# Performance work log

Hardware: AMD Instinct MI355X
Metric: run time of the kernel (lower is better)

## Reference

```python
import jax, jax.numpy as jnp
import numpy as np

DIM = 512
NUM_HEADS = 8
HEAD_DIM = DIM // NUM_HEADS
SCALE = HEAD_DIM ** -0.5


def setup_inputs() -> dict:
    key = jax.random.key(0)
    ks = jax.random.split(key, 11)
    B, T, D = 2, 4096, DIM
    s = 0.02
    return {
        "query": jax.random.normal(ks[0], (B, T, D), jnp.float32),
        "key_": jax.random.normal(ks[1], (B, T, D), jnp.float32),
        "value": jax.random.normal(ks[2], (B, T, D), jnp.float32),
        "Wq": jax.random.normal(ks[3], (D, D), jnp.float32) * s,
        "bq": jnp.zeros((D,), jnp.float32),
        "Wk": jax.random.normal(ks[4], (D, D), jnp.float32) * s,
        "bk": jnp.zeros((D,), jnp.float32),
        "Wv": jax.random.normal(ks[5], (D, D), jnp.float32) * s,
        "bv": jnp.zeros((D,), jnp.float32),
        "Wo": jax.random.normal(ks[6], (D, D), jnp.float32) * s,
        "bo": jnp.zeros((D,), jnp.float32),
    }


def reference(query, key_, value, Wq, bq, Wk, bk, Wv, bv, Wo, bo):
    B, T, D = query.shape
    H, Hd = NUM_HEADS, HEAD_DIM
    # Linear projections (torch Linear: x @ W.T + b)
    q = (query @ Wq.T + bq).reshape(B, T, H, Hd).transpose(0, 2, 1, 3)   # [B,H,T,Hd]
    k = (key_ @ Wk.T + bk).reshape(B, -1, H, Hd).transpose(0, 2, 1, 3)    # [B,H,S,Hd]
    v = (value @ Wv.T + bv).reshape(B, -1, H, Hd).transpose(0, 2, 1, 3)   # [B,H,S,Hd]
    # Full O(T*S) score matrix, as in the original (non-fused) module
    scores = jnp.einsum("bhtd,bhsd->bhts", q, k) * SCALE                  # [B,H,T,S]
    weights = jax.nn.softmax(scores, axis=-1)
    out = jnp.einsum("bhts,bhsd->bhtd", weights, v)                       # [B,H,T,Hd]
    out = out.transpose(0, 2, 1, 3).reshape(B, T, D)
    return out @ Wo.T + bo
```

## Files before the change

### kernel.cpp

```cpp
#include <hip/hip_runtime.h>
#include <cstdint>
#include <cstddef>

typedef __attribute__((ext_vector_type(8)))  __bf16 bf16x8;
typedef __attribute__((ext_vector_type(4)))  float  f32x4;
typedef __attribute__((ext_vector_type(16))) float  f32x16;
typedef __attribute__((ext_vector_type(8)))  unsigned short us8;

#define MFMA(a, b, c)   __builtin_amdgcn_mfma_f32_16x16x32_bf16((a), (b), (c), 0, 0, 0)
#define MFMA32(a, b, c) __builtin_amdgcn_mfma_f32_32x32x16_bf16((a), (b), (c), 0, 0, 0)

#define QSCALE 0.18033688011112042f

__device__ __forceinline__ unsigned short f2bf(float f) {
  unsigned u = __float_as_uint(f);
  u += 0x7fffu + ((u >> 16) & 1u);
  return (unsigned short)(u >> 16);
}

__device__ __forceinline__ float bf2f(unsigned short s) {
  unsigned u = ((unsigned)s) << 16;
  return __uint_as_float(u);
}

__device__ __forceinline__ unsigned cvtpk(float lo, float hi) {
  unsigned r;
  asm("v_cvt_pk_bf16_f32 %0, %1, %2" : "=v"(r) : "v"(lo), "v"(hi));
  return r;
}

__device__ __forceinline__ void pl32swap(unsigned& a, unsigned& b) {
  asm("v_permlane32_swap_b32 %0, %1" : "+v"(a), "+v"(b));
}

__device__ __forceinline__ void gload16(const void* g, void* l) {
  __builtin_amdgcn_global_load_lds(
      (__attribute__((address_space(1))) unsigned int*)(uintptr_t)g,
      (__attribute__((address_space(3))) unsigned int*)l,
      16, 0, 0);
}

__device__ __forceinline__ float tree16(const float* p) {
  float a = (p[0] + p[1]) + (p[2] + p[3]);
  float b = (p[4] + p[5]) + (p[6] + p[7]);
  float c = (p[8] + p[9]) + (p[10] + p[11]);
  float d = (p[12] + p[13]) + (p[14] + p[15]);
  return (a + b) + (c + d);
}

struct CastArgs {
  const float*    src[7];
  unsigned short* dst[7];
  int             n4[7];
};
__global__ __launch_bounds__(256) void cast_kernel(CastArgs a) {
  int z = blockIdx.y;
  const float* __restrict__ in = a.src[z];
  unsigned short* __restrict__ out = a.dst[z];
  int i = blockIdx.x * 256 + threadIdx.x;
  if (i < a.n4[z]) {
    float4 f = ((const float4*)in)[i];
    ushort4 r;
    r.x = f2bf(f.x); r.y = f2bf(f.y); r.z = f2bf(f.z); r.w = f2bf(f.w);
    ((ushort4*)out)[i] = r;
  }
}

struct ProjArgs {
  const unsigned short* X[3];
  const unsigned short* W[3];
  const float*          bias[3];
  unsigned short*       out[3];
};

__global__ __launch_bounds__(256) void proj_qkv_kernel(ProjArgs args) {
  __shared__ alignas(16) unsigned short smem[16384];

  const int z = blockIdx.z;
  const unsigned short* __restrict__ X   = args.X[z];
  const unsigned short* __restrict__ W   = args.W[z];
  const float* __restrict__ bias         = args.bias[z];
  unsigned short* __restrict__ out       = args.out[z];
  const float scl = (z == 0) ? QSCALE : 1.0f;

  const int t = threadIdx.x;
  const int w = t >> 6, lane = t & 63;
  const int quad = lane >> 4, l15 = lane & 15;
  const int wr = w >> 1, wc = w & 1;
  const int m0 = blockIdx.x * 128, n0 = blockIdx.y * 128;

  const int srow = t >> 2;
  const int scol = (((t & 3) ^ (srow & 3)) << 3);

  f32x4 acc[4][4] = {};

  {
    unsigned short* sA = smem;
    unsigned short* sB = smem + 4096;
    gload16(X + (size_t)(m0 + srow) * 512 + scol,      &sA[w * 512]);
    gload16(X + (size_t)(m0 + srow + 64) * 512 + scol, &sA[2048 + w * 512]);
    gload16(W + (size_t)(n0 + srow) * 512 + scol,      &sB[w * 512]);
    gload16(W + (size_t)(n0 + srow + 64) * 512 + scol, &sB[2048 + w * 512]);
  }

  for (int k0 = 0; k0 < 512; k0 += 32) {
    const int buf = (k0 >> 5) & 1;
    unsigned short* sA = smem + buf * 8192;
    unsigned short* sB = sA + 4096;
    if (k0 < 480) {
      unsigned short* nA = smem + (buf ^ 1) * 8192;
      unsigned short* nB = nA + 4096;
      const int kn = k0 + 32;
      gload16(X + (size_t)(m0 + srow) * 512 + kn + scol,      &nA[w * 512]);
      gload16(X + (size_t)(m0 + srow + 64) * 512 + kn + scol, &nA[2048 + w * 512]);
      gload16(W + (size_t)(n0 + srow) * 512 + kn + scol,      &nB[w * 512]);
      gload16(W + (size_t)(n0 + srow + 64) * 512 + kn + scol, &nB[2048 + w * 512]);
      asm volatile("s_waitcnt vmcnt(4)" ::: "memory");
    } else {
      asm volatile("s_waitcnt vmcnt(0)" ::: "memory");
    }
    __builtin_amdgcn_s_barrier();
    asm volatile("" ::: "memory");

    bf16x8 af[4], bfr[4];
#pragma unroll
    for (int mt = 0; mt < 4; ++mt) {
      int ra = wr * 64 + mt * 16 + l15;
      af[mt] = *(const bf16x8*)&sA[ra * 32 + ((quad ^ (ra & 3)) << 3)];
    }
#pragma unroll
    for (int nt = 0; nt < 4; ++nt) {
      int rb = wc * 64 + nt * 16 + l15;
      bfr[nt] = *(const bf16x8*)&sB[rb * 32 + ((quad ^ (rb & 3)) << 3)];
    }
#pragma unroll
    for (int mt = 0; mt < 4; ++mt)
#pragma unroll
      for (int nt = 0; nt < 4; ++nt)
        acc[mt][nt] = MFMA(af[mt], bfr[nt], acc[mt][nt]);

    asm volatile("" ::: "memory");
    __builtin_amdgcn_s_barrier();
  }

  if (z != 2) {
#pragma unroll
    for (int nt = 0; nt < 4; ++nt) {
      int n = n0 + wc * 64 + nt * 16 + l15;
      float bv = bias[n];
      int h = n >> 6, hd = n & 63;
#pragma unroll
      for (int mt = 0; mt < 4; ++mt) {
#pragma unroll
        for (int r = 0; r < 4; ++r) {
          int m = m0 + wr * 64 + mt * 16 + quad * 4 + r;
          int b = m >> 12, tt = m & 4095;
          out[(((size_t)(b * 8 + h)) * 4096 + tt) * 64 + hd] =
              f2bf((acc[mt][nt][r] + bv) * scl);
        }
      }
    }
  } else {
    const int b   = m0 >> 12;
    const int tt0 = m0 & 4095;
#pragma unroll
    for (int h2 = 0; h2 < 2; ++h2) {
      __syncthreads();
      if (wc == h2) {
#pragma unroll
        for (int nt = 0; nt < 4; ++nt) {
          int nl = nt * 16 + l15;
          float bv = bias[n0 + h2 * 64 + nl];
#pragma unroll
          for (int mt = 0; mt < 4; ++mt)
#pragma unroll
            for (int r = 0; r < 4; ++r) {
              int ml = wr * 64 + mt * 16 + quad * 4 + r;
              smem[nl * 136 + ml] = f2bf((acc[mt][nt][r] + bv) * scl);
            }
        }
      }
      __syncthreads();
      const int row = t >> 2;
      const int c4  = (t & 3) * 8;
      const int n   = n0 + h2 * 64 + row;
      unsigned short* dst = out + ((size_t)(b * 512 + n)) * 4096 + tt0;
#pragma unroll
      for (int k = 0; k < 4; ++k)
        *(us8*)(dst + c4 + k * 32) = *(const us8*)&smem[row * 136 + c4 + k * 32];
    }
  }
}

__global__ __launch_bounds__(256) void proj_out_kernel(
    const unsigned short* __restrict__ P0, const unsigned short* __restrict__ P1,
    const float* __restrict__ pL, const unsigned short* __restrict__ W,
    const float* __restrict__ bias, float* __restrict__ out) {
  __shared__ alignas(16) unsigned short sA[2][2048];
  __shared__ alignas(16) unsigned short sB[2][4096];
  __shared__ float invL[512];

  const int t = threadIdx.x;
  const int w = t >> 6, lane = t & 63;
  const int quad = lane >> 4, l15 = lane & 15;
  const int m0 = blockIdx.x * 64, n0 = blockIdx.y * 128;
  const int b  = m0 >> 12, tt0 = m0 & 4095;

  {
    const int hh = t >> 5;
    const int r2 = (t & 31) * 2;
#pragma unroll
    for (int i = 0; i < 2; ++i) {
      const int row = r2 + i;
      const size_t ix = (size_t)(b * 8 + hh) * 4096 + tt0 + row;
      invL[hh * 64 + row] = 1.0f / (pL[ix] + pL[65536 + ix]);
    }
  }

  const int arow = t >> 2, ac = t & 3;
  const int srow = t >> 2;
  const int scol = (((t & 3) ^ (srow & 3)) << 3);

  __syncthreads();

  {
    us8 a0 = *(const us8*)&P0[(size_t)(m0 + arow) * 512 + ac * 8];
    us8 a1 = *(const us8*)&P1[(size_t)(m0 + arow) * 512 + ac * 8];
    const float inv = invL[arow];
    unsigned o[4];
#pragma unroll
    for (int i = 0; i < 4; ++i)
      o[i] = cvtpk((bf2f(a0[2 * i]) + bf2f(a1[2 * i])) * inv,
                   (bf2f(a0[2 * i + 1]) + bf2f(a1[2 * i + 1])) * inv);
    *(us8*)&sA[0][arow * 32 + ((ac ^ (arow & 3)) << 3)] = *(us8*)o;
    gload16(W + (size_t)(n0 + srow) * 512 + scol,      &sB[0][w * 512]);
    gload16(W + (size_t)(n0 + srow + 64) * 512 + scol, &sB[0][2048 + w * 512]);
  }
  __syncthreads();

  f32x4 acc[4][2] = {};

  for (int k0 = 0; k0 < 512; k0 += 32) {
    const int buf = (k0 >> 5) & 1;

    us8 a0n = {}, a1n = {};
    float invn = 0.f;
    if (k0 < 480) {
      const int kn = k0 + 32;
      a0n = *(const us8*)&P0[(size_t)(m0 + arow) * 512 + kn + ac * 8];
      a1n = *(const us8*)&P1[(size_t)(m0 + arow) * 512 + kn + ac * 8];
      invn = invL[(kn >> 6) * 64 + arow];
      gload16(W + (size_t)(n0 + srow) * 512 + kn + scol,      &sB[buf ^ 1][w * 512]);
      gload16(W + (size_t)(n0 + srow + 64) * 512 + kn + scol, &sB[buf ^ 1][2048 + w * 512]);
    }

    bf16x8 af[4], bfr[2];
#pragma unroll
    for (int mt = 0; mt < 4; ++mt) {
      int ra = mt * 16 + l15;
      af[mt] = *(const bf16x8*)&sA[buf][ra * 32 + ((quad ^ (ra & 3)) << 3)];
    }
#pragma unroll
    for (int nt = 0; nt < 2; ++nt) {
      int rb = w * 32 + nt * 16 + l15;
      bfr[nt] = *(const bf16x8*)&sB[buf][rb * 32 + ((quad ^ (rb & 3)) << 3)];
    }
#pragma unroll
    for (int mt = 0; mt < 4; ++mt)
#pragma unroll
      for (int nt = 0; nt < 2; ++nt)
        acc[mt][nt] = MFMA(af[mt], bfr[nt], acc[mt][nt]);

    if (k0 < 480) {
      unsigned o[4];
#pragma unroll
      for (int i = 0; i < 4; ++i)
        o[i] = cvtpk((bf2f(a0n[2 * i]) + bf2f(a1n[2 * i])) * invn,
                     (bf2f(a0n[2 * i + 1]) + bf2f(a1n[2 * i + 1])) * invn);
      *(us8*)&sA[buf ^ 1][arow * 32 + ((ac ^ (arow & 3)) << 3)] = *(us8*)o;
    }

    asm volatile("s_waitcnt vmcnt(0) lgkmcnt(0)" ::: "memory");
    __builtin_amdgcn_s_barrier();
  }

#pragma unroll
  for (int nt = 0; nt < 2; ++nt) {
    int n = n0 + w * 32 + nt * 16 + l15;
    float bv = bias[n];
#pragma unroll
    for (int mt = 0; mt < 4; ++mt) {
#pragma unroll
      for (int r = 0; r < 4; ++r) {
        int m = m0 + mt * 16 + quad * 4 + r;
        out[(size_t)m * 512 + n] = acc[mt][nt][r] + bv;
      }
    }
  }
}

__global__ __launch_bounds__(128, 2) void attn_kernel(
    const unsigned short* __restrict__ Q, const unsigned short* __restrict__ K,
    const unsigned short* __restrict__ VT,
    unsigned short* __restrict__ pO0, unsigned short* __restrict__ pO1,
    float* __restrict__ pL) {
  __shared__ alignas(16) unsigned short kt[2][4096];
  __shared__ alignas(16) unsigned short vt[2][4096];

  const int t = threadIdx.x;
  const int w = t >> 6;
  const int lane = t & 63;
  const int l31 = lane & 31, h = lane >> 5;

  const int wg  = blockIdx.x + gridDim.x * blockIdx.y;
  const int swz = (wg & 7) * 128 + (wg >> 3);
  const int qt  = swz & 31;
  const int bh2 = swz >> 5;
  const int bh  = bh2 & 15, half = bh2 >> 4;

  const unsigned short* __restrict__ Qp  = Q  + (size_t)bh * 4096 * 64;
  const unsigned short* __restrict__ Kp  = K  + (size_t)bh * 4096 * 64;
  const unsigned short* __restrict__ VTp = VT + (size_t)bh * 64 * 4096;

  const int q0w = qt * 128 + w * 64;
  const int sbase = half * 2048;

  const int lr   = lane >> 3;
  const int gcol = (((lane & 7) ^ lr) << 3);

#define STAGE(bbuf, s0)                                                        \
  {                                                                            \
    _Pragma("unroll")                                                          \
    for (int i = 0; i < 4; ++i)                                                \
      gload16(Kp + (size_t)((s0) + w * 32 + i * 8 + lr) * 64 + gcol,           \
              &kt[bbuf][(w * 32 + i * 8) * 64]);                               \
    _Pragma("unroll")                                                          \
    for (int i = 0; i < 4; ++i)                                                \
      gload16(VTp + (size_t)(w * 32 + i * 8 + lr) * 4096 + (s0) + gcol,        \
              &vt[bbuf][(w * 32 + i * 8) * 64]);                               \
  }

  STAGE(0, sbase);

  bf16x8 aqA[4], aqB[4];
#pragma unroll
  for (int kd = 0; kd < 4; ++kd) {
    aqA[kd] = *(const bf16x8*)(Qp + (size_t)(q0w + l31) * 64 + kd * 16 + h * 8);
    aqB[kd] = *(const bf16x8*)(Qp + (size_t)(q0w + 32 + l31) * 64 + kd * 16 + h * 8);
  }

  f32x16 o0a = {}, o1a = {}, o0b = {}, o1b = {};
  float lia = 0.f, lib = 0.f;

  const int swzk = l31 & 7;

  for (int j = 0; j < 32; ++j) {
    const int cb = j & 1, nb = cb ^ 1;
    if (j < 31) {
      STAGE(nb, sbase + (j + 1) * 64);
      asm volatile("s_waitcnt vmcnt(8)" ::: "memory");
    } else {
      asm volatile("s_waitcnt vmcnt(0)" ::: "memory");
    }
    __builtin_amdgcn_s_barrier();
    asm volatile("" ::: "memory");

    const unsigned short* ktb = kt[cb];
    const unsigned short* vtb = vt[cb];

#pragma unroll
    for (int st = 0; st < 2; ++st) {
      bf16x8 kf[4];
#pragma unroll
      for (int kd = 0; kd < 4; ++kd)
        kf[kd] = *(const bf16x8*)&ktb[(st * 32 + l31) * 64 +
                                      (((2 * kd + h) ^ swzk) << 3)];
      f32x16 sa = {}, sb = {};
#pragma unroll
      for (int kd = 0; kd < 4; ++kd) {
        sa = MFMA32(kf[kd], aqA[kd], sa);
        sb = MFMA32(kf[kd], aqB[kd], sb);
      }

      float pA[16], pB[16];
#pragma unroll
      for (int r = 0; r < 16; ++r) {
        pA[r] = __builtin_amdgcn_exp2f(sa[r]);
        pB[r] = __builtin_amdgcn_exp2f(sb[r]);
      }
      lia += tree16(pA);
      lib += tree16(pB);

      unsigned XgA[4], YgA[4], XgB[4], YgB[4];
#pragma unroll
      for (int g = 0; g < 4; ++g) {
        XgA[g] = cvtpk(pA[4 * g + 0], pA[4 * g + 1]);
        YgA[g] = cvtpk(pA[4 * g + 2], pA[4 * g + 3]);
        XgB[g] = cvtpk(pB[4 * g + 0], pB[4 * g + 1]);
        YgB[g] = cvtpk(pB[4 * g + 2], pB[4 * g + 3]);
      }

#pragma unroll
      for (int ks = 0; ks < 2; ++ks) {
        const int c = st * 4 + 2 * ks + h;
        bf16x8 v0 = *(const bf16x8*)&vtb[l31 * 64 + ((c ^ swzk) << 3)];
        bf16x8 v1 = *(const bf16x8*)&vtb[(l31 + 32) * 64 + ((c ^ swzk) << 3)];

        unsigned a0 = XgA[2 * ks], a2 = XgA[2 * ks + 1];
        unsigned a1 = YgA[2 * ks], a3 = YgA[2 * ks + 1];
        pl32swap(a0, a2);
        pl32swap(a1, a3);
        union { unsigned u[4]; bf16x8 v; } paA;
        paA.u[0] = a0; paA.u[1] = a1; paA.u[2] = a2; paA.u[3] = a3;
        o0a = MFMA32(paA.v, v0, o0a);
        o1a = MFMA32(paA.v, v1, o1a);

        unsigned b0 = XgB[2 * ks], b2 = XgB[2 * ks + 1];
        unsigned b1 = YgB[2 * ks], b3 = YgB[2 * ks + 1];
        pl32swap(b0, b2);
        pl32swap(b1, b3);
        union { unsigned u[4]; bf16x8 v; } paB;
        paB.u[0] = b0; paB.u[1] = b1; paB.u[2] = b2; paB.u[3] = b3;
        o0b = MFMA32(paB.v, v0, o0b);
        o1b = MFMA32(paB.v, v1, o1b);
      }
    }

    asm volatile("" ::: "memory");
    __builtin_amdgcn_s_barrier();
  }
#undef STAGE

  lia += __shfl_xor(lia, 32, 64);
  lib += __shfl_xor(lib, 32, 64);
  float* __restrict__ PLh = pL + half * 65536 + bh * 4096;
  if (h == 0) {
    PLh[q0w + l31]      = lia;
    PLh[q0w + 32 + l31] = lib;
  }

  unsigned short* __restrict__ PO = half ? pO1 : pO0;
  const int bq = bh >> 3, hh = bh & 7;
#pragma unroll
  for (int r = 0; r < 16; ++r) {
    const int qloc = (r & 3) + 8 * (r >> 2) + 4 * h;
    const size_t baseA = ((size_t)bq * 4096 + q0w + qloc) * 512 + hh * 64;
    PO[baseA + l31]      = f2bf(o0a[r]);
    PO[baseA + 32 + l31] = f2bf(o1a[r]);
    const size_t baseB = ((size_t)bq * 4096 + q0w + 32 + qloc) * 512 + hh * 64;
    PO[baseB + l31]      = f2bf(o0b[r]);
    PO[baseB + 32 + l31] = f2bf(o1b[r]);
  }
}

extern "C" void kernel_launch(void* const* d_in, const int* in_sizes, int n_in,
                              void* d_out, int out_size, void* d_ws, size_t ws_size,
                              hipStream_t stream) {
  (void)in_sizes; (void)n_in; (void)out_size; (void)ws_size;
  const float* query = (const float*)d_in[0];
  const float* key_  = (const float*)d_in[1];
  const float* value = (const float*)d_in[2];
  const float* Wq = (const float*)d_in[3];
  const float* bq = (const float*)d_in[4];
  const float* Wk = (const float*)d_in[5];
  const float* bk = (const float*)d_in[6];
  const float* Wv = (const float*)d_in[7];
  const float* bv = (const float*)d_in[8];
  const float* Wo = (const float*)d_in[9];
  const float* bo = (const float*)d_in[10];
  float* out = (float*)d_out;

  char* ws = (char*)d_ws;
  const size_t MB = 1024 * 1024;
  unsigned short* Xq  = (unsigned short*)(ws + 0 * MB);
  unsigned short* Xk  = (unsigned short*)(ws + 8 * MB);
  unsigned short* Xv  = (unsigned short*)(ws + 16 * MB);
  unsigned short* Wqb = (unsigned short*)(ws + 24 * MB);
  unsigned short* Wkb = (unsigned short*)(ws + 24 * MB + 512 * 1024);
  unsigned short* Wvb = (unsigned short*)(ws + 25 * MB);
  unsigned short* qb  = (unsigned short*)(ws + 26 * MB);
  unsigned short* kb  = (unsigned short*)(ws + 34 * MB);
  unsigned short* vtb = (unsigned short*)(ws + 42 * MB);
  unsigned short* Wob = (unsigned short*)(ws + 58 * MB);
  unsigned short* pO0 = (unsigned short*)(ws + 0 * MB);
  unsigned short* pO1 = (unsigned short*)(ws + 9 * MB);
  float*          pL  = (float*)(ws + 18 * MB);

  CastArgs ca;
  ca.src[0] = query; ca.src[1] = key_; ca.src[2] = value;
  ca.src[3] = Wq;    ca.src[4] = Wk;   ca.src[5] = Wv;  ca.src[6] = Wo;
  ca.dst[0] = Xq;    ca.dst[1] = Xk;   ca.dst[2] = Xv;
  ca.dst[3] = Wqb;   ca.dst[4] = Wkb;  ca.dst[5] = Wvb; ca.dst[6] = Wob;
  ca.n4[0] = ca.n4[1] = ca.n4[2] = 1048576;
  ca.n4[3] = ca.n4[4] = ca.n4[5] = ca.n4[6] = 65536;
  cast_kernel<<<dim3(4096, 7), 256, 0, stream>>>(ca);

  ProjArgs pa;
  pa.X[0] = Xq;  pa.X[1] = Xk;  pa.X[2] = Xv;
  pa.W[0] = Wqb; pa.W[1] = Wkb; pa.W[2] = Wvb;
  pa.bias[0] = bq; pa.bias[1] = bk; pa.bias[2] = bv;
  pa.out[0] = qb; pa.out[1] = kb; pa.out[2] = vtb;
  proj_qkv_kernel<<<dim3(64, 4, 3), 256, 0, stream>>>(pa);

  attn_kernel<<<dim3(32, 32), 128, 0, stream>>>(qb, kb, vtb, pO0, pO1, pL);

  proj_out_kernel<<<dim3(128, 4), 256, 0, stream>>>(pO0, pO1, pL, Wob, bo, out);
}
```

Before: 220.0 us.

## Triple-buffer projection GEMM loads, compact cast grid, and prioritize attention MFMAs

The QKV and output projection kernels move from double to triple buffering of their LDS tiles, prefetching two k-steps ahead and loosening the vmcnt waits so global loads overlap more compute. The cast kernel's 2D grid, where most blocks for the small weight matrices had nothing to do, becomes a flat 1D grid of exactly the needed blocks. In the attention kernel, s_setprio is raised around the MFMA sections so waves issuing matrix ops get scheduling priority. These changes cost extra LDS per block, which may lower occupancy, and full unrolling of the k loops increases code size.

```diff
diff --git a/kernel.cpp b/kernel.cpp
--- a/kernel.cpp
+++ b/kernel.cpp
@@ -51,19 +51,16 @@
 struct CastArgs {
   const float*    src[7];
   unsigned short* dst[7];
-  int             n4[7];
 };
 __global__ __launch_bounds__(256) void cast_kernel(CastArgs a) {
-  int z = blockIdx.y;
-  const float* __restrict__ in = a.src[z];
-  unsigned short* __restrict__ out = a.dst[z];
-  int i = blockIdx.x * 256 + threadIdx.x;
-  if (i < a.n4[z]) {
-    float4 f = ((const float4*)in)[i];
-    ushort4 r;
-    r.x = f2bf(f.x); r.y = f2bf(f.y); r.z = f2bf(f.z); r.w = f2bf(f.w);
-    ((ushort4*)out)[i] = r;
-  }
+  const int i = blockIdx.x * 256 + threadIdx.x;
+  int z, off;
+  if (i < 3145728) { z = i >> 20;            off = i & 1048575; }
+  else             { int j = i - 3145728; z = 3 + (j >> 16); off = j & 65535; }
+  float4 f = ((const float4*)a.src[z])[off];
+  ushort4 r;
+  r.x = f2bf(f.x); r.y = f2bf(f.y); r.z = f2bf(f.z); r.w = f2bf(f.w);
+  ((ushort4*)a.dst[z])[off] = r;
 }
 
 struct ProjArgs {
@@ -74,7 +71,7 @@
 };
 
 __global__ __launch_bounds__(256) void proj_qkv_kernel(ProjArgs args) {
-  __shared__ alignas(16) unsigned short smem[16384];
+  __shared__ alignas(16) unsigned short smem[3 * 8192];
 
   const int z = blockIdx.z;
   const unsigned short* __restrict__ X   = args.X[z];
@@ -94,27 +91,28 @@
 
   f32x4 acc[4][4] = {};
 
-  {
-    unsigned short* sA = smem;
-    unsigned short* sB = smem + 4096;
-    gload16(X + (size_t)(m0 + srow) * 512 + scol,      &sA[w * 512]);
-    gload16(X + (size_t)(m0 + srow + 64) * 512 + scol, &sA[2048 + w * 512]);
-    gload16(W + (size_t)(n0 + srow) * 512 + scol,      &sB[w * 512]);
-    gload16(W + (size_t)(n0 + srow + 64) * 512 + scol, &sB[2048 + w * 512]);
-  }
-
+#define STAGEP(idx, kk)                                                        \
+  {                                                                            \
+    unsigned short* nA = smem + (idx) * 8192;                                  \
+    unsigned short* nB = nA + 4096;                                            \
+    gload16(X + (size_t)(m0 + srow) * 512 + (kk) + scol,      &nA[w * 512]);   \
+    gload16(X + (size_t)(m0 + srow + 64) * 512 + (kk) + scol, &nA[2048 + w * 512]); \
+    gload16(W + (size_t)(n0 + srow) * 512 + (kk) + scol,      &nB[w * 512]);   \
+    gload16(W + (size_t)(n0 + srow + 64) * 512 + (kk) + scol, &nB[2048 + w * 512]); \
+  }
+
+  STAGEP(0, 0);
+  STAGEP(1, 32);
+
+#pragma unroll
   for (int k0 = 0; k0 < 512; k0 += 32) {
-    const int buf = (k0 >> 5) & 1;
-    unsigned short* sA = smem + buf * 8192;
+    const int bi = (k0 >> 5) % 3;
+    unsigned short* sA = smem + bi * 8192;
     unsigned short* sB = sA + 4096;
-    if (k0 < 480) {
-      unsigned short* nA = smem + (buf ^ 1) * 8192;
-      unsigned short* nB = nA + 4096;
-      const int kn = k0 + 32;
-      gload16(X + (size_t)(m0 + srow) * 512 + kn + scol,      &nA[w * 512]);
-      gload16(X + (size_t)(m0 + srow + 64) * 512 + kn + scol, &nA[2048 + w * 512]);
-      gload16(W + (size_t)(n0 + srow) * 512 + kn + scol,      &nB[w * 512]);
-      gload16(W + (size_t)(n0 + srow + 64) * 512 + kn + scol, &nB[2048 + w * 512]);
+    if (k0 < 448) {
+      STAGEP((bi + 2) % 3, k0 + 64);
+      asm volatile("s_waitcnt vmcnt(8)" ::: "memory");
+    } else if (k0 == 448) {
       asm volatile("s_waitcnt vmcnt(4)" ::: "memory");
     } else {
       asm volatile("s_waitcnt vmcnt(0)" ::: "memory");
@@ -142,6 +140,7 @@
     asm volatile("" ::: "memory");
     __builtin_amdgcn_s_barrier();
   }
+#undef STAGEP
 
   if (z != 2) {
 #pragma unroll
@@ -197,7 +196,7 @@
     const float* __restrict__ pL, const unsigned short* __restrict__ W,
     const float* __restrict__ bias, float* __restrict__ out) {
   __shared__ alignas(16) unsigned short sA[2][2048];
-  __shared__ alignas(16) unsigned short sB[2][4096];
+  __shared__ alignas(16) unsigned short sB[3][4096];
   __shared__ float invL[512];
 
   const int t = threadIdx.x;
@@ -235,13 +234,17 @@
     *(us8*)&sA[0][arow * 32 + ((ac ^ (arow & 3)) << 3)] = *(us8*)o;
     gload16(W + (size_t)(n0 + srow) * 512 + scol,      &sB[0][w * 512]);
     gload16(W + (size_t)(n0 + srow + 64) * 512 + scol, &sB[0][2048 + w * 512]);
+    gload16(W + (size_t)(n0 + srow) * 512 + 32 + scol,      &sB[1][w * 512]);
+    gload16(W + (size_t)(n0 + srow + 64) * 512 + 32 + scol, &sB[1][2048 + w * 512]);
   }
   __syncthreads();
 
   f32x4 acc[4][2] = {};
 
+#pragma unroll
   for (int k0 = 0; k0 < 512; k0 += 32) {
-    const int buf = (k0 >> 5) & 1;
+    const int ba = (k0 >> 5) & 1;
+    const int bb = (k0 >> 5) % 3;
 
     us8 a0n = {}, a1n = {};
     float invn = 0.f;
@@ -250,20 +253,23 @@
       a0n = *(const us8*)&P0[(size_t)(m0 + arow) * 512 + kn + ac * 8];
       a1n = *(const us8*)&P1[(size_t)(m0 + arow) * 512 + kn + ac * 8];
       invn = invL[(kn >> 6) * 64 + arow];
-      gload16(W + (size_t)(n0 + srow) * 512 + kn + scol,      &sB[buf ^ 1][w * 512]);
-      gload16(W + (size_t)(n0 + srow + 64) * 512 + kn + scol, &sB[buf ^ 1][2048 + w * 512]);
+    }
+    if (k0 < 448) {
+      const int kn2 = k0 + 64;
+      gload16(W + (size_t)(n0 + srow) * 512 + kn2 + scol,      &sB[(bb + 2) % 3][w * 512]);
+      gload16(W + (size_t)(n0 + srow + 64) * 512 + kn2 + scol, &sB[(bb + 2) % 3][2048 + w * 512]);
     }
 
     bf16x8 af[4], bfr[2];
 #pragma unroll
     for (int mt = 0; mt < 4; ++mt) {
       int ra = mt * 16 + l15;
-      af[mt] = *(const bf16x8*)&sA[buf][ra * 32 + ((quad ^ (ra & 3)) << 3)];
+      af[mt] = *(const bf16x8*)&sA[ba][ra * 32 + ((quad ^ (ra & 3)) << 3)];
     }
 #pragma unroll
     for (int nt = 0; nt < 2; ++nt) {
       int rb = w * 32 + nt * 16 + l15;
-      bfr[nt] = *(const bf16x8*)&sB[buf][rb * 32 + ((quad ^ (rb & 3)) << 3)];
+      bfr[nt] = *(const bf16x8*)&sB[bb][rb * 32 + ((quad ^ (rb & 3)) << 3)];
     }
 #pragma unroll
     for (int mt = 0; mt < 4; ++mt)
@@ -277,10 +283,10 @@
       for (int i = 0; i < 4; ++i)
         o[i] = cvtpk((bf2f(a0n[2 * i]) + bf2f(a1n[2 * i])) * invn,
                      (bf2f(a0n[2 * i + 1]) + bf2f(a1n[2 * i + 1])) * invn);
-      *(us8*)&sA[buf ^ 1][arow * 32 + ((ac ^ (arow & 3)) << 3)] = *(us8*)o;
-    }
-
-    asm volatile("s_waitcnt vmcnt(0) lgkmcnt(0)" ::: "memory");
+      *(us8*)&sA[ba ^ 1][arow * 32 + ((ac ^ (arow & 3)) << 3)] = *(us8*)o;
+    }
+
+    asm volatile("s_waitcnt vmcnt(2) lgkmcnt(0)" ::: "memory");
     __builtin_amdgcn_s_barrier();
   }
 
@@ -376,11 +382,13 @@
         kf[kd] = *(const bf16x8*)&ktb[(st * 32 + l31) * 64 +
                                       (((2 * kd + h) ^ swzk) << 3)];
       f32x16 sa = {}, sb = {};
+      __builtin_amdgcn_s_setprio(1);
 #pragma unroll
       for (int kd = 0; kd < 4; ++kd) {
         sa = MFMA32(kf[kd], aqA[kd], sa);
         sb = MFMA32(kf[kd], aqB[kd], sb);
       }
+      __builtin_amdgcn_s_setprio(0);
 
       float pA[16], pB[16];
 #pragma unroll
@@ -400,6 +408,7 @@
         YgB[g] = cvtpk(pB[4 * g + 2], pB[4 * g + 3]);
       }
 
+      __builtin_amdgcn_s_setprio(1);
 #pragma unroll
       for (int ks = 0; ks < 2; ++ks) {
         const int c = st * 4 + 2 * ks + h;
@@ -424,6 +433,7 @@
         o0b = MFMA32(paB.v, v0, o0b);
         o1b = MFMA32(paB.v, v1, o1b);
       }
+      __builtin_amdgcn_s_setprio(0);
     }
 
     asm volatile("" ::: "memory");
@@ -491,9 +501,7 @@
   ca.src[3] = Wq;    ca.src[4] = Wk;   ca.src[5] = Wv;  ca.src[6] = Wo;
   ca.dst[0] = Xq;    ca.dst[1] = Xk;   ca.dst[2] = Xv;
   ca.dst[3] = Wqb;   ca.dst[4] = Wkb;  ca.dst[5] = Wvb; ca.dst[6] = Wob;
-  ca.n4[0] = ca.n4[1] = ca.n4[2] = 1048576;
-  ca.n4[3] = ca.n4[4] = ca.n4[5] = ca.n4[6] = 65536;
-  cast_kernel<<<dim3(4096, 7), 256, 0, stream>>>(ca);
+  cast_kernel<<<dim3(13312), 256, 0, stream>>>(ca);
 
   ProjArgs pa;
   pa.X[0] = Xq;  pa.X[1] = Xk;  pa.X[2] = Xv;
```

After: 219.6 us. No clear change (-0.2%).
